# Kernel optimization log

Measured on AMD Instinct MI355X. Metric: run time of the kernel, lower is better.

Reference implementation:

```python
import jax, jax.numpy as jnp
import numpy as np

D_MODEL = 1024
NUM_HEADS = 16
HEAD_DIM = D_MODEL // NUM_HEADS


def setup_inputs() -> dict:
    key = jax.random.key(0)
    k_x, k_wqkv, k_bqkv, k_wo, k_bo = jax.random.split(key, 5)
    s = 1.0 / np.sqrt(D_MODEL)
    return {
        "x": jax.random.normal(k_x, (4, 2048, D_MODEL), dtype=jnp.float32),
        "W_qkv": jax.random.uniform(k_wqkv, (D_MODEL, 3 * D_MODEL), jnp.float32, -s, s),
        "b_qkv": jax.random.uniform(k_bqkv, (3 * D_MODEL,), jnp.float32, -s, s),
        "W_out": jax.random.uniform(k_wo, (D_MODEL, D_MODEL), jnp.float32, -s, s),
        "b_out": jax.random.uniform(k_bo, (D_MODEL,), jnp.float32, -s, s),
    }


def reference(x, W_qkv, b_qkv, W_out, b_out):
    B, N, C = x.shape
    # fused QKV projection -> [B, N, 3, H, Dh]
    qkv = (x @ W_qkv + b_qkv).reshape(B, N, 3, NUM_HEADS, HEAD_DIM)
    q = jnp.transpose(qkv[:, :, 0], (0, 2, 1, 3))  # [B, H, N, Dh]
    k = jnp.transpose(qkv[:, :, 1], (0, 2, 1, 3))
    v = jnp.transpose(qkv[:, :, 2], (0, 2, 1, 3))
    scale = 1.0 / jnp.sqrt(jnp.asarray(HEAD_DIM, dtype=x.dtype))
    attn = jnp.einsum('bhqd,bhkd->bhqk', q, k) * scale  # [B, H, N, N]
    attn = jax.nn.softmax(attn, axis=-1)
    # dropout is identity in eval mode
    out = jnp.einsum('bhqk,bhkd->bhqd', attn, v)  # [B, H, N, Dh]
    out = jnp.transpose(out, (0, 2, 1, 3)).reshape(B, N, C)
    return out @ W_out + b_out
```

## Files before the change

kernel.cpp:

```cpp
#include <hip/hip_runtime.h>


typedef __bf16 bf16x8 __attribute__((ext_vector_type(8)));
typedef float f32x4 __attribute__((ext_vector_type(4)));
typedef unsigned int u32x4 __attribute__((ext_vector_type(4)));

#define DEV __device__ __forceinline__

DEV unsigned short f2b(float x) {
  unsigned int u = __float_as_uint(x);
  u += 0x7fffu + ((u >> 16) & 1u);
  return (unsigned short)(u >> 16);
}

DEV unsigned int pk2(float a, float b) {
  union { __bf16 h[2]; unsigned int u; } c;
  c.h[0] = (__bf16)a;
  c.h[1] = (__bf16)b;
  return c.u;
}

#if __has_builtin(__builtin_amdgcn_exp2f)
DEV float exp2_fast(float x) { return __builtin_amdgcn_exp2f(x); }
#else
DEV float exp2_fast(float x) { return exp2f(x); }
#endif

DEV void xpose_pair(unsigned int a, unsigned int b,
                    unsigned int& x, unsigned int& y) {
#if __has_builtin(__builtin_amdgcn_permlane32_swap) && \
    __has_builtin(__builtin_amdgcn_permlane16_swap)
  auto t = __builtin_amdgcn_permlane32_swap(a, b, false, false);
  auto u = __builtin_amdgcn_permlane16_swap(t[0], t[1], false, false);
  x = u[0];
  y = u[1];
#else
  int la = (int)(threadIdx.x & 63);
  unsigned int a32 = (unsigned int)__shfl_xor((int)a, 32, 64);
  unsigned int b32 = (unsigned int)__shfl_xor((int)b, 32, 64);
  unsigned int t0 = (la < 32) ? a : b32;
  unsigned int t1 = (la < 32) ? a32 : b;
  unsigned int t0x = (unsigned int)__shfl_xor((int)t0, 16, 64);
  unsigned int t1x = (unsigned int)__shfl_xor((int)t1, 16, 64);
  bool odd = ((la >> 4) & 1) != 0;
  x = odd ? t1x : t0;
  y = odd ? t1 : t0x;
#endif
}

DEV bf16x8 u4_to_bf(u32x4 v) {
  union { u32x4 u; bf16x8 b; } c;
  c.u = v;
  return c.b;
}

DEV void g2l16(const void* g, void* l) {
  __builtin_amdgcn_global_load_lds(
      (const __attribute__((address_space(1))) unsigned int*)(unsigned long long)g,
      (__attribute__((address_space(3))) unsigned int*)(unsigned int)(unsigned long long)l,
      16, 0, 0);
}

__global__ void cvt_x_kernel(const float* __restrict__ x,
                             unsigned short* __restrict__ xb) {
  int i = blockIdx.x * blockDim.x + threadIdx.x;
  float4 v = ((const float4*)x)[i];
  ushort4 o;
  o.x = f2b(v.x); o.y = f2b(v.y); o.z = f2b(v.z); o.w = f2b(v.w);
  ((ushort4*)xb)[i] = o;
}

__global__ void cvt_wt_kernel(const float* __restrict__ W,
                              unsigned short* __restrict__ Wt,
                              int K, int N) {
  __shared__ float tile[32][33];
  int n0 = blockIdx.x * 32, k0 = blockIdx.y * 32;
  int tx = threadIdx.x, ty = threadIdx.y;
#pragma unroll
  for (int i = 0; i < 32; i += 8)
    tile[ty + i][tx] = W[(size_t)(k0 + ty + i) * N + n0 + tx];
  __syncthreads();
#pragma unroll
  for (int i = 0; i < 32; i += 8)
    Wt[(size_t)(n0 + ty + i) * K + k0 + tx] = f2b(tile[tx][ty + i]);
}

#define QSCALE 0.18033688011112042f

template <int MODE>
__global__ __launch_bounds__(256, 2)
void gemm_bt_kernel(const unsigned short* __restrict__ A,
                    const unsigned short* __restrict__ Bt,
                    const float* __restrict__ bias,
                    unsigned short* __restrict__ qout,
                    unsigned short* __restrict__ kfrout,
                    unsigned short* __restrict__ vfrout,
                    float* __restrict__ fout) {
  constexpr int K = 1024;
  __shared__ unsigned short As[128 * 32];
  __shared__ unsigned short Bs[128 * 32];

  const int tid = threadIdx.x;
  const int lane = tid & 63;
  const int w = tid >> 6;
  const int wm = w & 1, wn = w >> 1;
  const int l15 = lane & 15, quad = lane >> 4;
  const int m0 = blockIdx.y * 128;
  const int n0 = blockIdx.x * 128;

  const unsigned short* Ag = A + (size_t)m0 * K;
  const unsigned short* Bg = Bt + (size_t)n0 * K;

  const int c0 = tid, c1 = tid + 256;
  const size_t ga0 = (size_t)(c0 >> 2) * K + (size_t)(c0 & 3) * 8;
  const size_t ga1 = (size_t)(c1 >> 2) * K + (size_t)(c1 & 3) * 8;
  unsigned short* la0 = &As[c0 * 8];
  unsigned short* la1 = &As[c1 * 8];
  unsigned short* lb0 = &Bs[c0 * 8];
  unsigned short* lb1 = &Bs[c1 * 8];

  f32x4 acc[4][4] = {};

  for (int kt = 0; kt < K; kt += 32) {
    g2l16(Ag + ga0 + kt, la0);
    g2l16(Ag + ga1 + kt, la1);
    g2l16(Bg + ga0 + kt, lb0);
    g2l16(Bg + ga1 + kt, lb1);
    __syncthreads();
    bf16x8 af[4], bfr[4];
#pragma unroll
    for (int i = 0; i < 4; ++i) {
      af[i]  = *(const bf16x8*)&As[(wm * 64 + i * 16 + l15) * 32 + quad * 8];
      bfr[i] = *(const bf16x8*)&Bs[(wn * 64 + i * 16 + l15) * 32 + quad * 8];
    }
#pragma unroll
    for (int mi = 0; mi < 4; ++mi)
#pragma unroll
      for (int ni = 0; ni < 4; ++ni)
        acc[mi][ni] = __builtin_amdgcn_mfma_f32_16x16x32_bf16(
            af[mi], bfr[ni], acc[mi][ni], 0, 0, 0);
    __syncthreads();
  }

  float bv[4];
#pragma unroll
  for (int ni = 0; ni < 4; ++ni)
    bv[ni] = bias[n0 + wn * 64 + ni * 16 + l15];

  if (MODE == 0) {
    const int sel = n0 >> 10;
    const int bbat = m0 >> 11;
    const int ktb = ((m0 & 2047) >> 6) + wm;
    if (sel == 0) {
#pragma unroll
      for (int mi = 0; mi < 4; ++mi) {
        int rb = m0 + wm * 64 + mi * 16 + quad * 4;
#pragma unroll
        for (int ni = 0; ni < 4; ++ni) {
          int c = (n0 & 1023) + wn * 64 + ni * 16 + l15;
#pragma unroll
          for (int r = 0; r < 4; ++r)
            qout[(size_t)(rb + r) * 1024 + c] =
                f2b((acc[mi][ni][r] + bv[ni]) * QSCALE);
        }
      }
    } else if (sel == 1) {
#pragma unroll
      for (int ni = 0; ni < 4; ++ni) {
        int c = (n0 & 1023) + wn * 64 + ni * 16 + l15;
        int h = c >> 6, d = c & 63;
        int kc = d >> 5, dq = (d >> 3) & 3, j = d & 7;
        size_t fb = ((((size_t)(bbat * 16 + h) * 32 + ktb) * 8) + kc) * 512 +
                    (size_t)(dq * 16) * 8 + j;
#pragma unroll
        for (int mi = 0; mi < 4; ++mi) {
          size_t fm = fb + (size_t)mi * 1024;
#pragma unroll
          for (int r = 0; r < 4; ++r)
            kfrout[fm + (quad * 4 + r) * 8] = f2b(acc[mi][ni][r] + bv[ni]);
        }
      }
    } else {
      const int fqb = quad >> 1;
      const int jj0 = (quad & 1) * 4;
#pragma unroll
      for (int ni = 0; ni < 4; ++ni) {
        int c = (n0 & 1023) + wn * 64 + ni * 16 + l15;
        int h = c >> 6, d = c & 63;
        int df = d >> 4, fl15 = d & 15;
#pragma unroll
        for (int mi = 0; mi < 4; ++mi) {
          int kc2 = mi >> 1;
          int fquad = (mi & 1) * 2 + fqb;
          size_t fb = ((((size_t)(bbat * 16 + h) * 32 + ktb) * 8) + df * 2 + kc2) * 512 +
                      (size_t)(fquad * 16 + fl15) * 8 + jj0;
          ushort4 pk;
          pk.x = f2b(acc[mi][ni][0] + bv[ni]);
          pk.y = f2b(acc[mi][ni][1] + bv[ni]);
          pk.z = f2b(acc[mi][ni][2] + bv[ni]);
          pk.w = f2b(acc[mi][ni][3] + bv[ni]);
          *(ushort4*)&vfrout[fb] = pk;
        }
      }
    }
  } else {
#pragma unroll
    for (int mi = 0; mi < 4; ++mi) {
      int rb = m0 + wm * 64 + mi * 16 + quad * 4;
#pragma unroll
      for (int ni = 0; ni < 4; ++ni) {
        int c = n0 + wn * 64 + ni * 16 + l15;
#pragma unroll
        for (int r = 0; r < 4; ++r)
          fout[(size_t)(rb + r) * 1024 + c] = acc[mi][ni][r] + bv[ni];
      }
    }
  }
}

__global__ __launch_bounds__(256, 2)
void attn_kernel(const unsigned short* __restrict__ qg,
                 const unsigned short* __restrict__ kfr,
                 const unsigned short* __restrict__ vfr,
                 unsigned short* __restrict__ oat) {
  __shared__ unsigned short Ks[2][4096];
  __shared__ unsigned short Vs[2][4096];

  const int tid = threadIdx.x;
  const int lane = tid & 63;
  const int w = tid >> 6;
  const int l15 = lane & 15, quad = lane >> 4;

  const int head = blockIdx.x * 8 + (blockIdx.y >> 3);
  const int q0 = (blockIdx.y & 7) * 256 + w * 64;
  const int b = head >> 4, h = head & 15;
  const size_t tokbase = (size_t)b * 2048;

  bf16x8 qf[4][2];
#pragma unroll
  for (int ni = 0; ni < 4; ++ni)
#pragma unroll
    for (int kc = 0; kc < 2; ++kc) {
      int q = q0 + ni * 16 + l15;
      qf[ni][kc] = *(const bf16x8*)(qg + (tokbase + q) * 1024 + h * 64 +
                                    kc * 32 + quad * 8);
    }

  f32x4 oacc[4][4] = {};
  float lsum[4] = {0.f, 0.f, 0.f, 0.f};

  const unsigned short* kpb = kfr + (size_t)head * 32 * 4096;
  const unsigned short* vpb = vfr + (size_t)head * 32 * 4096;

  auto stage = [&](int buf, int t) {
    const unsigned short* ks = kpb + (size_t)t * 4096;
    const unsigned short* vs = vpb + (size_t)t * 4096;
    g2l16(ks + (size_t)tid * 8,         &Ks[buf][tid * 8]);
    g2l16(ks + (size_t)(tid + 256) * 8, &Ks[buf][(tid + 256) * 8]);
    g2l16(vs + (size_t)tid * 8,         &Vs[buf][tid * 8]);
    g2l16(vs + (size_t)(tid + 256) * 8, &Vs[buf][(tid + 256) * 8]);
  };

  stage(0, 0);
  __syncthreads();

  const f32x4 z4 = {0.f, 0.f, 0.f, 0.f};

  for (int t = 0; t < 32; ++t) {
    const int cur = t & 1;
    if (t < 31) stage(cur ^ 1, t + 1);

    const unsigned short* Kb = Ks[cur];
    bf16x8 kf[8];
#pragma unroll
    for (int f = 0; f < 8; ++f)
      kf[f] = *(const bf16x8*)&Kb[f * 512 + lane * 8];

    f32x4 st[2][4];
    bf16x8 pf2[4][2];
    __builtin_amdgcn_s_setprio(1);
#pragma unroll
    for (int mi = 0; mi < 4; ++mi)
      st[0][mi] = __builtin_amdgcn_mfma_f32_16x16x32_bf16(
          kf[mi * 2], qf[0][0], z4, 0, 0, 0);
#pragma unroll
    for (int mi = 0; mi < 4; ++mi)
      st[0][mi] = __builtin_amdgcn_mfma_f32_16x16x32_bf16(
          kf[mi * 2 + 1], qf[0][1], st[0][mi], 0, 0, 0);
    __builtin_amdgcn_s_setprio(0);

#pragma unroll
    for (int ni = 0; ni < 4; ++ni) {
      const int pcur = ni & 1, pnx = pcur ^ 1;
      if (ni < 3) {
        __builtin_amdgcn_s_setprio(1);
#pragma unroll
        for (int mi = 0; mi < 4; ++mi)
          st[pnx][mi] = __builtin_amdgcn_mfma_f32_16x16x32_bf16(
              kf[mi * 2], qf[ni + 1][0], z4, 0, 0, 0);
#pragma unroll
        for (int mi = 0; mi < 4; ++mi)
          st[pnx][mi] = __builtin_amdgcn_mfma_f32_16x16x32_bf16(
              kf[mi * 2 + 1], qf[ni + 1][1], st[pnx][mi], 0, 0, 0);
        __builtin_amdgcn_s_setprio(0);
      }
      float rs = 0.f;
      unsigned int s0[4], s1[4];
#pragma unroll
      for (int mi = 0; mi < 4; ++mi) {
        float p0 = exp2_fast(st[pcur][mi][0]);
        float p1 = exp2_fast(st[pcur][mi][1]);
        float p2 = exp2_fast(st[pcur][mi][2]);
        float p3 = exp2_fast(st[pcur][mi][3]);
        rs += (p0 + p1) + (p2 + p3);
        s0[mi] = pk2(p0, p1);
        s1[mi] = pk2(p2, p3);
      }
      lsum[ni] += rs;
      unsigned int o00, o01, o02, o03, o10, o11, o12, o13;
      xpose_pair(s0[0], s0[1], o00, o02);
      xpose_pair(s1[0], s1[1], o01, o03);
      xpose_pair(s0[2], s0[3], o10, o12);
      xpose_pair(s1[2], s1[3], o11, o13);
      u32x4 t0 = {o00, o01, o02, o03};
      u32x4 t1 = {o10, o11, o12, o13};
      pf2[ni][0] = u4_to_bf(t0);
      pf2[ni][1] = u4_to_bf(t1);
    }

    const unsigned short* Vb = Vs[cur];
#pragma unroll
    for (int kc = 0; kc < 2; ++kc) {
      bf16x8 vf4[4];
#pragma unroll
      for (int df = 0; df < 4; ++df)
        vf4[df] = *(const bf16x8*)&Vb[(df * 2 + kc) * 512 + lane * 8];
      __builtin_amdgcn_s_setprio(1);
#pragma unroll
      for (int df = 0; df < 4; ++df)
#pragma unroll
        for (int ni = 0; ni < 4; ++ni)
          oacc[df][ni] = __builtin_amdgcn_mfma_f32_16x16x32_bf16(
              vf4[df], pf2[ni][kc], oacc[df][ni], 0, 0, 0);
      __builtin_amdgcn_s_setprio(0);
    }

    if (t < 31) __syncthreads();
  }

#pragma unroll
  for (int ni = 0; ni < 4; ++ni) {
    float s = lsum[ni];
    s += __shfl_xor(s, 16, 64);
    s += __shfl_xor(s, 32, 64);
    float inv = __builtin_amdgcn_rcpf(s);
    int q = q0 + ni * 16 + l15;
#pragma unroll
    for (int df = 0; df < 4; ++df) {
      uint2 pw;
      pw.x = pk2(oacc[df][ni][0] * inv, oacc[df][ni][1] * inv);
      pw.y = pk2(oacc[df][ni][2] * inv, oacc[df][ni][3] * inv);
      *(uint2*)&oat[(tokbase + q) * 1024 + h * 64 + df * 16 + quad * 4] = pw;
    }
  }
}

extern "C" void kernel_launch(void* const* d_in, const int* in_sizes, int n_in,
                              void* d_out, int out_size, void* d_ws, size_t ws_size,
                              hipStream_t stream) {
  const float* x    = (const float*)d_in[0];
  const float* Wqkv = (const float*)d_in[1];
  const float* bqkv = (const float*)d_in[2];
  const float* Wout = (const float*)d_in[3];
  const float* bout = (const float*)d_in[4];
  float* out = (float*)d_out;

  char* ws = (char*)d_ws;
  unsigned short* xb  = (unsigned short*)(ws + (size_t)0);
  unsigned short* wqt = (unsigned short*)(ws + ((size_t)16 << 20));
  unsigned short* wot = (unsigned short*)(ws + ((size_t)22 << 20));
  unsigned short* qbf = (unsigned short*)(ws + ((size_t)24 << 20));
  unsigned short* kfr = (unsigned short*)(ws + ((size_t)40 << 20));
  unsigned short* vfr = (unsigned short*)(ws + ((size_t)56 << 20));
  unsigned short* oat = (unsigned short*)(ws + ((size_t)72 << 20));

  cvt_x_kernel<<<8192, 256, 0, stream>>>(x, xb);
  cvt_wt_kernel<<<dim3(96, 32), dim3(32, 8), 0, stream>>>(Wqkv, wqt, 1024, 3072);
  cvt_wt_kernel<<<dim3(32, 32), dim3(32, 8), 0, stream>>>(Wout, wot, 1024, 1024);

  gemm_bt_kernel<0><<<dim3(24, 64), 256, 0, stream>>>(
      xb, wqt, bqkv, qbf, kfr, vfr, nullptr);

  attn_kernel<<<dim3(8, 64), 256, 0, stream>>>(qbf, kfr, vfr, oat);

  gemm_bt_kernel<1><<<dim3(8, 64), 256, 0, stream>>>(
      oat, wot, bout, nullptr, nullptr, nullptr, out);
}
```

Before: 279.7 us.

## Warp-specialize attention into QK/softmax producer and PV consumer waves

The attention kernel grows to 512 threads. Four waves compute QK^T and exp, then write bf16 P tiles and row sums into double-buffered LDS. The other four waves run the PV MFMAs one tile behind and do the final normalization and store. The goal is to overlap the exp/transpose work with the PV matrix multiplies on different waves. The cost is an extra LDS round trip for P, more LDS use, one block per CU, and a block-wide barrier every tile.

After: 290.8 us. +4.0%, slower.

```diff
diff --git a/kernel.cpp b/kernel.cpp
--- a/kernel.cpp
+++ b/kernel.cpp
@@ -218,149 +218,156 @@
   }
 }
 
-__global__ __launch_bounds__(256, 2)
+__global__ __launch_bounds__(512, 1)
 void attn_kernel(const unsigned short* __restrict__ qg,
                  const unsigned short* __restrict__ kfr,
                  const unsigned short* __restrict__ vfr,
                  unsigned short* __restrict__ oat) {
   __shared__ unsigned short Ks[2][4096];
   __shared__ unsigned short Vs[2][4096];
+  __shared__ unsigned short Pb[2][4 * 4096];
+  __shared__ float lsumLDS[256];
 
   const int tid = threadIdx.x;
   const int lane = tid & 63;
   const int w = tid >> 6;
   const int l15 = lane & 15, quad = lane >> 4;
+  const int sub = w & 3;
 
   const int head = blockIdx.x * 8 + (blockIdx.y >> 3);
-  const int q0 = (blockIdx.y & 7) * 256 + w * 64;
+  const int q0 = (blockIdx.y & 7) * 256;
   const int b = head >> 4, h = head & 15;
   const size_t tokbase = (size_t)b * 2048;
 
-  bf16x8 qf[4][2];
-#pragma unroll
-  for (int ni = 0; ni < 4; ++ni)
-#pragma unroll
-    for (int kc = 0; kc < 2; ++kc) {
-      int q = q0 + ni * 16 + l15;
-      qf[ni][kc] = *(const bf16x8*)(qg + (tokbase + q) * 1024 + h * 64 +
-                                    kc * 32 + quad * 8);
-    }
-
-  f32x4 oacc[4][4] = {};
-  float lsum[4] = {0.f, 0.f, 0.f, 0.f};
-
   const unsigned short* kpb = kfr + (size_t)head * 32 * 4096;
   const unsigned short* vpb = vfr + (size_t)head * 32 * 4096;
 
-  auto stage = [&](int buf, int t) {
-    const unsigned short* ks = kpb + (size_t)t * 4096;
-    const unsigned short* vs = vpb + (size_t)t * 4096;
-    g2l16(ks + (size_t)tid * 8,         &Ks[buf][tid * 8]);
-    g2l16(ks + (size_t)(tid + 256) * 8, &Ks[buf][(tid + 256) * 8]);
-    g2l16(vs + (size_t)tid * 8,         &Vs[buf][tid * 8]);
-    g2l16(vs + (size_t)(tid + 256) * 8, &Vs[buf][(tid + 256) * 8]);
+  auto stageK = [&](int buf, int t) {
+    g2l16(kpb + (size_t)t * 4096 + tid * 8, &Ks[buf][tid * 8]);
   };
-
-  stage(0, 0);
+  auto stageV = [&](int buf, int t) {
+    g2l16(vpb + (size_t)t * 4096 + tid * 8, &Vs[buf][tid * 8]);
+  };
+
+  const f32x4 z4 = {0.f, 0.f, 0.f, 0.f};
+
+  stageK(0, 0);
   __syncthreads();
 
-  const f32x4 z4 = {0.f, 0.f, 0.f, 0.f};
-
-  for (int t = 0; t < 32; ++t) {
-    const int cur = t & 1;
-    if (t < 31) stage(cur ^ 1, t + 1);
-
-    const unsigned short* Kb = Ks[cur];
-    bf16x8 kf[8];
-#pragma unroll
-    for (int f = 0; f < 8; ++f)
-      kf[f] = *(const bf16x8*)&Kb[f * 512 + lane * 8];
-
-    f32x4 st[2][4];
-    bf16x8 pf2[4][2];
-    __builtin_amdgcn_s_setprio(1);
-#pragma unroll
-    for (int mi = 0; mi < 4; ++mi)
-      st[0][mi] = __builtin_amdgcn_mfma_f32_16x16x32_bf16(
-          kf[mi * 2], qf[0][0], z4, 0, 0, 0);
-#pragma unroll
-    for (int mi = 0; mi < 4; ++mi)
-      st[0][mi] = __builtin_amdgcn_mfma_f32_16x16x32_bf16(
-          kf[mi * 2 + 1], qf[0][1], st[0][mi], 0, 0, 0);
-    __builtin_amdgcn_s_setprio(0);
+  if (w < 4) {
+    bf16x8 qf[4][2];
+#pragma unroll
+    for (int ni = 0; ni < 4; ++ni)
+#pragma unroll
+      for (int kc = 0; kc < 2; ++kc) {
+        int q = q0 + sub * 64 + ni * 16 + l15;
+        qf[ni][kc] = *(const bf16x8*)(qg + (tokbase + q) * 1024 + h * 64 +
+                                      kc * 32 + quad * 8);
+      }
+    float lsum[4] = {0.f, 0.f, 0.f, 0.f};
+
+    for (int t = 0; t < 32; ++t) {
+      if (t < 31) stageK((t + 1) & 1, t + 1);
+      stageV(t & 1, t);
+
+      const unsigned short* Kb = Ks[t & 1];
+      bf16x8 kf[8];
+#pragma unroll
+      for (int f = 0; f < 8; ++f)
+        kf[f] = *(const bf16x8*)&Kb[f * 512 + lane * 8];
+
+      unsigned short* Pw = &Pb[t & 1][sub * 4096];
+#pragma unroll
+      for (int ni = 0; ni < 4; ++ni) {
+        f32x4 st[4];
+#pragma unroll
+        for (int mi = 0; mi < 4; ++mi)
+          st[mi] = __builtin_amdgcn_mfma_f32_16x16x32_bf16(
+              kf[mi * 2], qf[ni][0], z4, 0, 0, 0);
+#pragma unroll
+        for (int mi = 0; mi < 4; ++mi)
+          st[mi] = __builtin_amdgcn_mfma_f32_16x16x32_bf16(
+              kf[mi * 2 + 1], qf[ni][1], st[mi], 0, 0, 0);
+
+        float rs = 0.f;
+        unsigned int s0[4], s1[4];
+#pragma unroll
+        for (int mi = 0; mi < 4; ++mi) {
+          float p0 = exp2_fast(st[mi][0]);
+          float p1 = exp2_fast(st[mi][1]);
+          float p2 = exp2_fast(st[mi][2]);
+          float p3 = exp2_fast(st[mi][3]);
+          rs += (p0 + p1) + (p2 + p3);
+          s0[mi] = pk2(p0, p1);
+          s1[mi] = pk2(p2, p3);
+        }
+        lsum[ni] += rs;
+        unsigned int o00, o01, o02, o03, o10, o11, o12, o13;
+        xpose_pair(s0[0], s0[1], o00, o02);
+        xpose_pair(s1[0], s1[1], o01, o03);
+        xpose_pair(s0[2], s0[3], o10, o12);
+        xpose_pair(s1[2], s1[3], o11, o13);
+        u32x4 t0 = {o00, o01, o02, o03};
+        u32x4 t1 = {o10, o11, o12, o13};
+        *(bf16x8*)&Pw[(ni * 2 + 0) * 512 + lane * 8] = u4_to_bf(t0);
+        *(bf16x8*)&Pw[(ni * 2 + 1) * 512 + lane * 8] = u4_to_bf(t1);
+      }
+      __syncthreads();
+    }
 
 #pragma unroll
     for (int ni = 0; ni < 4; ++ni) {
-      const int pcur = ni & 1, pnx = pcur ^ 1;
-      if (ni < 3) {
-        __builtin_amdgcn_s_setprio(1);
-#pragma unroll
-        for (int mi = 0; mi < 4; ++mi)
-          st[pnx][mi] = __builtin_amdgcn_mfma_f32_16x16x32_bf16(
-              kf[mi * 2], qf[ni + 1][0], z4, 0, 0, 0);
-#pragma unroll
-        for (int mi = 0; mi < 4; ++mi)
-          st[pnx][mi] = __builtin_amdgcn_mfma_f32_16x16x32_bf16(
-              kf[mi * 2 + 1], qf[ni + 1][1], st[pnx][mi], 0, 0, 0);
-        __builtin_amdgcn_s_setprio(0);
-      }
-      float rs = 0.f;
-      unsigned int s0[4], s1[4];
-#pragma unroll
-      for (int mi = 0; mi < 4; ++mi) {
-        float p0 = exp2_fast(st[pcur][mi][0]);
-        float p1 = exp2_fast(st[pcur][mi][1]);
-        float p2 = exp2_fast(st[pcur][mi][2]);
-        float p3 = exp2_fast(st[pcur][mi][3]);
-        rs += (p0 + p1) + (p2 + p3);
-        s0[mi] = pk2(p0, p1);
-        s1[mi] = pk2(p2, p3);
-      }
-      lsum[ni] += rs;
-      unsigned int o00, o01, o02, o03, o10, o11, o12, o13;
-      xpose_pair(s0[0], s0[1], o00, o02);
-      xpose_pair(s1[0], s1[1], o01, o03);
-      xpose_pair(s0[2], s0[3], o10, o12);
-      xpose_pair(s1[2], s1[3], o11, o13);
-      u32x4 t0 = {o00, o01, o02, o03};
-      u32x4 t1 = {o10, o11, o12, o13};
-      pf2[ni][0] = u4_to_bf(t0);
-      pf2[ni][1] = u4_to_bf(t1);
-    }
-
-    const unsigned short* Vb = Vs[cur];
-#pragma unroll
-    for (int kc = 0; kc < 2; ++kc) {
-      bf16x8 vf4[4];
-#pragma unroll
-      for (int df = 0; df < 4; ++df)
-        vf4[df] = *(const bf16x8*)&Vb[(df * 2 + kc) * 512 + lane * 8];
-      __builtin_amdgcn_s_setprio(1);
-#pragma unroll
-      for (int df = 0; df < 4; ++df)
-#pragma unroll
-        for (int ni = 0; ni < 4; ++ni)
+      float s = lsum[ni];
+      s += __shfl_xor(s, 16, 64);
+      s += __shfl_xor(s, 32, 64);
+      if (quad == 0) lsumLDS[sub * 64 + ni * 16 + l15] = s;
+    }
+    __syncthreads();
+  } else {
+    f32x4 oacc[4][4] = {};
+
+    auto doPV = [&](int pb) {
+      const unsigned short* Vb = Vs[pb];
+      bf16x8 vf[8];
+#pragma unroll
+      for (int f = 0; f < 8; ++f)
+        vf[f] = *(const bf16x8*)&Vb[f * 512 + lane * 8];
+      const unsigned short* Pr = &Pb[pb][sub * 4096];
+#pragma unroll
+      for (int ni = 0; ni < 4; ++ni) {
+        bf16x8 p0 = *(const bf16x8*)&Pr[(ni * 2 + 0) * 512 + lane * 8];
+        bf16x8 p1 = *(const bf16x8*)&Pr[(ni * 2 + 1) * 512 + lane * 8];
+#pragma unroll
+        for (int df = 0; df < 4; ++df)
           oacc[df][ni] = __builtin_amdgcn_mfma_f32_16x16x32_bf16(
-              vf4[df], pf2[ni][kc], oacc[df][ni], 0, 0, 0);
-      __builtin_amdgcn_s_setprio(0);
-    }
-
-    if (t < 31) __syncthreads();
-  }
-
-#pragma unroll
-  for (int ni = 0; ni < 4; ++ni) {
-    float s = lsum[ni];
-    s += __shfl_xor(s, 16, 64);
-    s += __shfl_xor(s, 32, 64);
-    float inv = __builtin_amdgcn_rcpf(s);
-    int q = q0 + ni * 16 + l15;
-#pragma unroll
-    for (int df = 0; df < 4; ++df) {
-      uint2 pw;
-      pw.x = pk2(oacc[df][ni][0] * inv, oacc[df][ni][1] * inv);
-      pw.y = pk2(oacc[df][ni][2] * inv, oacc[df][ni][3] * inv);
-      *(uint2*)&oat[(tokbase + q) * 1024 + h * 64 + df * 16 + quad * 4] = pw;
+              vf[df * 2], p0, oacc[df][ni], 0, 0, 0);
+#pragma unroll
+        for (int df = 0; df < 4; ++df)
+          oacc[df][ni] = __builtin_amdgcn_mfma_f32_16x16x32_bf16(
+              vf[df * 2 + 1], p1, oacc[df][ni], 0, 0, 0);
+      }
+    };
+
+    for (int t = 0; t < 32; ++t) {
+      if (t < 31) stageK((t + 1) & 1, t + 1);
+      stageV(t & 1, t);
+      if (t > 0) doPV((t - 1) & 1);
+      __syncthreads();
+    }
+    doPV(1);
+    __syncthreads();
+
+#pragma unroll
+    for (int ni = 0; ni < 4; ++ni) {
+      float inv = __builtin_amdgcn_rcpf(lsumLDS[sub * 64 + ni * 16 + l15]);
+      int q = q0 + sub * 64 + ni * 16 + l15;
+#pragma unroll
+      for (int df = 0; df < 4; ++df) {
+        uint2 pw;
+        pw.x = pk2(oacc[df][ni][0] * inv, oacc[df][ni][1] * inv);
+        pw.y = pk2(oacc[df][ni][2] * inv, oacc[df][ni][3] * inv);
+        *(uint2*)&oat[(tokbase + q) * 1024 + h * 64 + df * 16 + quad * 4] = pw;
+      }
     }
   }
 }
@@ -391,7 +398,7 @@
   gemm_bt_kernel<0><<<dim3(24, 64), 256, 0, stream>>>(
       xb, wqt, bqkv, qbf, kfr, vfr, nullptr);
 
-  attn_kernel<<<dim3(8, 64), 256, 0, stream>>>(qbf, kfr, vfr, oat);
+  attn_kernel<<<dim3(8, 64), 512, 0, stream>>>(qbf, kfr, vfr, oat);
 
   gemm_bt_kernel<1><<<dim3(8, 64), 256, 0, stream>>>(
       oat, wot, bout, nullptr, nullptr, nullptr, out);
```
